# Kernel tuning notes

Hardware: AMD Instinct MI355X
Metric: run time of the kernel (lower is better)

## Reference

```python
import jax, jax.numpy as jnp
import numpy as np

WIN = 7           # window height/width
DIM = 192         # channels
HEADS = 6
HEAD_DIM = DIM // HEADS  # 32
B_WIN = 4096      # num_windows * batch
NW = 64           # windows per image (for shift mask)
N = WIN * WIN     # 49 tokens per window
THETA = 10.0


def _init_rope_freqs(key):
    # init_random_2d_freqs: mag = 1/theta^(arange(0,hd,4)[:hd//4]/hd)
    mag = 1.0 / THETA ** (jnp.arange(0, HEAD_DIM, 4)[: HEAD_DIM // 4].astype(jnp.float32) / HEAD_DIM)
    ang = jax.random.uniform(key, (HEADS, 1)) * 2.0 * jnp.pi
    fx = jnp.concatenate([mag * jnp.cos(ang), mag * jnp.cos(jnp.pi / 2 + ang)], axis=-1)  # [H, hd/2]
    fy = jnp.concatenate([mag * jnp.sin(ang), mag * jnp.sin(jnp.pi / 2 + ang)], axis=-1)
    return jnp.stack([fx, fy], axis=0)  # [2, H, hd/2]


def setup_inputs() -> dict:
    key = jax.random.key(0)
    ks = jax.random.split(key, 6)
    x = jax.random.normal(ks[0], (B_WIN, N, DIM), dtype=jnp.float32)
    mask = jnp.zeros((NW, N, N), dtype=jnp.float32)  # 0/-inf shift mask (zeros: no shift)
    qkv_w = jax.random.normal(ks[1], (3 * DIM, DIM), dtype=jnp.float32) * 0.02
    qkv_b = jnp.zeros((3 * DIM,), dtype=jnp.float32)
    proj_w = jax.random.normal(ks[2], (DIM, DIM), dtype=jnp.float32) * 0.02
    proj_b = jnp.zeros((DIM,), dtype=jnp.float32)
    rope_freqs = _init_rope_freqs(ks[3])
    return {"x": x, "mask": mask, "qkv_w": qkv_w, "qkv_b": qkv_b,
            "proj_w": proj_w, "proj_b": proj_b, "rope_freqs": rope_freqs}


def _rope_angles(rope_freqs):
    # t_x = t % end_x, t_y = t // end_x over the flattened window grid
    t = jnp.arange(N, dtype=jnp.float32)
    t_x = jnp.mod(t, WIN)
    t_y = jnp.floor_divide(t, WIN)
    # angle[h, n, d] = t_x[n]*fx[h,d] + t_y[n]*fy[h,d]  -> [H, N, hd/2]
    ang = (t_x[None, :, None] * rope_freqs[0][:, None, :]
           + t_y[None, :, None] * rope_freqs[1][:, None, :])
    return jnp.cos(ang), jnp.sin(ang)


def _apply_rope(u, cos, sin):
    # u: [B, H, N, hd]; complex multiply on (even, odd) pairs
    b, h, n, d = u.shape
    ur = u.reshape(b, h, n, d // 2, 2)
    re = ur[..., 0] * cos - ur[..., 1] * sin
    im = ur[..., 0] * sin + ur[..., 1] * cos
    return jnp.stack([re, im], axis=-1).reshape(b, h, n, d)


def reference(x, mask, qkv_w, qkv_b, proj_w, proj_b, rope_freqs):
    B_, n, C = x.shape
    H, hd = HEADS, HEAD_DIM
    scale = hd ** -0.5
    qkv = (x @ qkv_w.T + qkv_b).reshape(B_, n, 3, H, hd)
    qkv = jnp.transpose(qkv, (2, 0, 3, 1, 4))          # [3, B, H, N, hd]
    q, k, v = qkv[0] * scale, qkv[1], qkv[2]
    cos, sin = _rope_angles(rope_freqs)                 # [H, N, hd/2]
    q = _apply_rope(q, cos, sin)
    k = _apply_rope(k, cos, sin)
    attn = jnp.einsum('bhnd,bhmd->bhnm', q, k)          # [B, H, N, N]
    nW = mask.shape[0]
    attn = attn.reshape(B_ // nW, nW, H, n, n) + mask[None, :, None]
    attn = jax.nn.softmax(attn.reshape(B_, H, n, n), axis=-1)
    out = jnp.einsum('bhnm,bhmd->bhnd', attn, v)        # [B, H, N, hd]
    out = jnp.transpose(out, (0, 2, 1, 3)).reshape(B_, n, C)
    return out @ proj_w.T + proj_b
```

## Files before the change

kernel.cpp:

```cpp
#include <hip/hip_runtime.h>

#define NTOK 49
#define DIM 192
#define HEADS 6
#define NWIN 64
#define NBLK 4096

typedef unsigned short u16;
typedef short bf16x8 __attribute__((ext_vector_type(8)));
typedef unsigned short u16x4 __attribute__((ext_vector_type(4)));
typedef unsigned short u16x8 __attribute__((ext_vector_type(8)));
typedef float f32x4 __attribute__((ext_vector_type(4)));

#define QKVW_ELEMS (3 * DIM * DIM)
#define PROJW_ELEMS (DIM * DIM)

#define TB_OFF_BYTES ((QKVW_ELEMS + PROJW_ELEMS) * 2)
#define TB_QUADS     (HEADS * NTOK * 8)

#define R1_OFF 0
#define K_OFF  24576
#define PS_OFF 44176
#define LDS_TOTAL 51232

__device__ __forceinline__ float bf2f(u16 u) {
    union { unsigned int i; float f; } x; x.i = ((unsigned int)u) << 16; return x.f;
}
__device__ __forceinline__ u16 f2bf(float f) {
    union { float f; unsigned int u; } x; x.f = f;
    unsigned int u = x.u;
    u += 0x7fffu + ((u >> 16) & 1u);
    return (u16)(u >> 16);
}

extern "C" __global__ void __launch_bounds__(256)
convert_weights(const float* __restrict__ qkv_w, const float* __restrict__ proj_w,
                u16* __restrict__ ws) {
    int i = (blockIdx.x * 256 + threadIdx.x) * 4;
    if (i >= QKVW_ELEMS + PROJW_ELEMS) return;
    const float* s = (i < QKVW_ELEMS) ? (qkv_w + i) : (proj_w + (i - QKVW_ELEMS));
    float4 v = *(const float4*)s;
    ushort4 o;
    o.x = f2bf(v.x); o.y = f2bf(v.y); o.z = f2bf(v.z); o.w = f2bf(v.w);
    *(ushort4*)(ws + i) = o;
}

extern "C" __global__ void __launch_bounds__(256)
rope_table(const float* __restrict__ rfreq, float* __restrict__ tb) {
    int i = blockIdx.x * 256 + threadIdx.x;
    if (i >= TB_QUADS) return;
    int h = i / (NTOK * 8);
    int r = i % (NTOK * 8);
    int t = r >> 3;
    int p0 = (r & 7) * 2;
    float tx = (float)(t % 7), ty = (float)(t / 7);
    float a0 = tx * rfreq[h * 16 + p0]     + ty * rfreq[96 + h * 16 + p0];
    float a1 = tx * rfreq[h * 16 + p0 + 1] + ty * rfreq[96 + h * 16 + p0 + 1];
    float4 o;
    o.x = cosf(a0); o.y = sinf(a0);
    o.z = cosf(a1); o.w = sinf(a1);
    ((float4*)tb)[i] = o;
}

extern "C" __global__ void __launch_bounds__(256, 3)
fused_win_attn(const float* __restrict__ x, const float* __restrict__ mask,
               const u16* __restrict__ wsq, const float* __restrict__ qkv_b,
               const u16* __restrict__ wsp, const float* __restrict__ proj_b,
               const float* __restrict__ tb, float* __restrict__ out)
{
    __shared__ __align__(16) char smem[LDS_TOTAL];
    u16* xs = (u16*)(smem + R1_OFF);
    u16* qs = (u16*)(smem + R1_OFF);
    u16* vt = (u16*)(smem + R1_OFF);
    u16* kb = (u16*)(smem + K_OFF);
    u16* ps = (u16*)(smem + PS_OFF);

    const int tid  = threadIdx.x;
    const int wave = tid >> 6;
    const int lane = tid & 63;
    const int ln   = lane & 15;
    const int quad = lane >> 4;
    const int blk  = blockIdx.x;
    const int widx = blk & (NWIN - 1);
    const float* xg = x + (long)blk * NTOK * DIM;
    const f32x4 fzero = {0.f, 0.f, 0.f, 0.f};
    const float scale = 0.17677669529663687f;

    float mreg[4][4];
    #pragma unroll
    for (int nt = 0; nt < 4; nt++) {
        int m = nt * 16 + ln;
        #pragma unroll
        for (int r = 0; r < 4; r++) {
            int n = wave * 16 + quad * 4 + r;
            mreg[nt][r] = (m >= NTOK) ? -1e30f
                         : ((n < NTOK) ? mask[widx * (NTOK * NTOK) + n * NTOK + m] : 0.f);
        }
    }

    for (int i = tid; i < NTOK * 48; i += 256) {
        int r = i / 48, c = (i % 48) * 4;
        float4 v = *(const float4*)(xg + r * DIM + c);
        u16x4 o = { f2bf(v.x), f2bf(v.y), f2bf(v.z), f2bf(v.w) };
        *(u16x4*)(xs + r * 200 + c) = o;
    }
    __syncthreads();

    bf16x8 bfrag[6][4];
    #pragma unroll
    for (int kk = 0; kk < 6; kk++)
        #pragma unroll
        for (int nt = 0; nt < 4; nt++) {
            int row = nt * 16 + ln; if (row > NTOK - 1) row = NTOK - 1;
            bfrag[kk][nt] = *(const bf16x8*)(xs + row * 200 + kk * 32 + quad * 8);
        }
    __syncthreads();

    for (int jt = wave; jt < 24; jt += 4) {
        bf16x8 af[6];
        const u16* wr = wsq + (jt * 16 + ln) * DIM + quad * 8;
        #pragma unroll
        for (int kk = 0; kk < 6; kk++) af[kk] = *(const bf16x8*)(wr + kk * 32);
        f32x4 acc[4];
        #pragma unroll
        for (int nt = 0; nt < 4; nt++) acc[nt] = fzero;
        #pragma unroll
        for (int kk = 0; kk < 6; kk++)
            #pragma unroll
            for (int nt = 0; nt < 4; nt++)
                acc[nt] = __builtin_amdgcn_mfma_f32_16x16x32_bf16(af[kk], bfrag[kk][nt], acc[nt], 0, 0, 0);

        int j0 = jt * 16 + quad * 4;
        int isq = (jt < 12);
        int c0 = j0 % DIM;
        int hh = c0 >> 5;
        int p0 = (c0 & 31) >> 1;
        float b0 = qkv_b[j0],   b1 = qkv_b[j0+1];
        float b2 = qkv_b[j0+2], b3 = qkv_b[j0+3];
        #pragma unroll
        for (int nt = 0; nt < 4; nt++) {
            int t = nt * 16 + ln;
            float v0 = acc[nt][0] + b0;
            float v1 = acc[nt][1] + b1;
            float v2 = acc[nt][2] + b2;
            float v3 = acc[nt][3] + b3;
            if (t < NTOK) {
                float4 tv = ((const float4*)tb)[(hh * NTOK + t) * 8 + (p0 >> 1)];
                float r0 = v0 * tv.x - v1 * tv.y;
                float i0 = v0 * tv.y + v1 * tv.x;
                float r1 = v2 * tv.z - v3 * tv.w;
                float i1 = v2 * tv.w + v3 * tv.z;
                if (isq) { r0 *= scale; i0 *= scale; r1 *= scale; i1 *= scale; }
                u16x4 pk = { f2bf(r0), f2bf(i0), f2bf(r1), f2bf(i1) };
                *(u16x4*)((isq ? qs : kb) + t * 200 + c0) = pk;
            }
        }
    }
    __syncthreads();

    bf16x8 qreg[6];
    {
        int qrow = wave * 16 + ln; if (qrow > NTOK - 1) qrow = NTOK - 1;
        #pragma unroll
        for (int h = 0; h < HEADS; h++)
            qreg[h] = *(const bf16x8*)(qs + qrow * 200 + h * 32 + quad * 8);
    }
    __syncthreads();

    for (int jt = 24 + wave; jt < 36; jt += 4) {
        bf16x8 af[6];
        const u16* wr = wsq + (jt * 16 + ln) * DIM + quad * 8;
        #pragma unroll
        for (int kk = 0; kk < 6; kk++) af[kk] = *(const bf16x8*)(wr + kk * 32);
        f32x4 acc[4];
        #pragma unroll
        for (int nt = 0; nt < 4; nt++) acc[nt] = fzero;
        #pragma unroll
        for (int kk = 0; kk < 6; kk++)
            #pragma unroll
            for (int nt = 0; nt < 4; nt++)
                acc[nt] = __builtin_amdgcn_mfma_f32_16x16x32_bf16(af[kk], bfrag[kk][nt], acc[nt], 0, 0, 0);

        int j0 = jt * 16 + quad * 4;
        int c0 = j0 - 2 * DIM;
        float b0 = qkv_b[j0],   b1 = qkv_b[j0+1];
        float b2 = qkv_b[j0+2], b3 = qkv_b[j0+3];
        #pragma unroll
        for (int nt = 0; nt < 4; nt++) {
            int t = nt * 16 + ln;
            float w0 = (t < NTOK) ? acc[nt][0] + b0 : 0.f;
            float w1 = (t < NTOK) ? acc[nt][1] + b1 : 0.f;
            float w2 = (t < NTOK) ? acc[nt][2] + b2 : 0.f;
            float w3 = (t < NTOK) ? acc[nt][3] + b3 : 0.f;
            vt[(c0+0) * 64 + (t ^ (((c0+0) & 7) << 3))] = f2bf(w0);
            vt[(c0+1) * 64 + (t ^ (((c0+1) & 7) << 3))] = f2bf(w1);
            vt[(c0+2) * 64 + (t ^ (((c0+2) & 7) << 3))] = f2bf(w2);
            vt[(c0+3) * 64 + (t ^ (((c0+3) & 7) << 3))] = f2bf(w3);
        }
    }
    __syncthreads();

    u16x4 op0[HEADS], op1[HEADS];
    #pragma unroll
    for (int h = 0; h < HEADS; h++) {
        f32x4 s4[4];
        #pragma unroll
        for (int nt = 0; nt < 4; nt++) {
            int krow = nt * 16 + ln; if (krow > NTOK - 1) krow = NTOK - 1;
            bf16x8 bk = *(const bf16x8*)(kb + krow * 200 + h * 32 + quad * 8);
            s4[nt] = __builtin_amdgcn_mfma_f32_16x16x32_bf16(qreg[h], bk, fzero, 0, 0, 0);
        }
        #pragma unroll
        for (int nt = 0; nt < 4; nt++)
            #pragma unroll
            for (int r = 0; r < 4; r++)
                s4[nt][r] += mreg[nt][r];
        float mx[4], sm[4], rs[4];
        #pragma unroll
        for (int r = 0; r < 4; r++) {
            float v = fmaxf(fmaxf(s4[0][r], s4[1][r]), fmaxf(s4[2][r], s4[3][r]));
            #pragma unroll
            for (int d = 1; d < 16; d <<= 1) v = fmaxf(v, __shfl_xor(v, d));
            mx[r] = v; sm[r] = 0.f;
        }
        #pragma unroll
        for (int nt = 0; nt < 4; nt++) {
            int m = nt * 16 + ln;
            #pragma unroll
            for (int r = 0; r < 4; r++) {
                float e = __expf(s4[nt][r] - mx[r]);
                sm[r] += e;
                int prow = wave * 16 + quad * 4 + r;
                if (prow < NTOK) ps[prow * 72 + m] = f2bf(e);
            }
        }
        #pragma unroll
        for (int r = 0; r < 4; r++) {
            float v = sm[r];
            #pragma unroll
            for (int d = 1; d < 16; d <<= 1) v += __shfl_xor(v, d);
            rs[r] = 1.0f / v;
        }
        f32x4 o0 = fzero, o1 = fzero;
        int arow = wave * 16 + ln; if (arow > NTOK - 1) arow = NTOK - 1;
        int swz = (ln & 7) << 3;
        #pragma unroll
        for (int kk = 0; kk < 2; kk++) {
            bf16x8 ap  = *(const bf16x8*)(ps + arow * 72 + kk * 32 + quad * 8);
            int cbase = (kk * 32 + quad * 8) ^ swz;
            bf16x8 bv0 = *(const bf16x8*)(vt + (h * 32 + ln) * 64      + cbase);
            bf16x8 bv1 = *(const bf16x8*)(vt + (h * 32 + 16 + ln) * 64 + cbase);
            o0 = __builtin_amdgcn_mfma_f32_16x16x32_bf16(ap, bv0, o0, 0, 0, 0);
            o1 = __builtin_amdgcn_mfma_f32_16x16x32_bf16(ap, bv1, o1, 0, 0, 0);
        }
        #pragma unroll
        for (int r = 0; r < 4; r++) {
            op0[h][r] = f2bf(o0[r] * rs[r]);
            op1[h][r] = f2bf(o1[r] * rs[r]);
        }
    }
    __syncthreads();

    #pragma unroll
    for (int h = 0; h < HEADS; h++)
        #pragma unroll
        for (int r = 0; r < 4; r++) {
            int t = wave * 16 + quad * 4 + r;
            if (t < NTOK) {
                kb[t * 200 + h * 32 + ln]      = op0[h][r];
                kb[t * 200 + h * 32 + 16 + ln] = op1[h][r];
            }
        }
    bf16x8 aa[6];
    int arow = wave * 16 + ln; if (arow > NTOK - 1) arow = NTOK - 1;
    #pragma unroll
    for (int kk = 0; kk < 6; kk++)
        aa[kk] = *(const bf16x8*)(kb + arow * 200 + kk * 32 + quad * 8);
    float* ob = out + (long)blk * (NTOK * DIM);
    for (int nt = 0; nt < 12; nt++) {
        const u16* wp = wsp + (nt * 16 + ln) * DIM + quad * 8;
        f32x4 p4 = fzero;
        #pragma unroll
        for (int kk = 0; kk < 6; kk++) {
            bf16x8 bw = *(const bf16x8*)(wp + kk * 32);
            p4 = __builtin_amdgcn_mfma_f32_16x16x32_bf16(aa[kk], bw, p4, 0, 0, 0);
        }
        float bb = proj_b[nt * 16 + ln];
        #pragma unroll
        for (int r = 0; r < 4; r++) {
            int t = wave * 16 + quad * 4 + r;
            if (t < NTOK) ob[t * DIM + nt * 16 + ln] = p4[r] + bb;
        }
    }
}

extern "C" void kernel_launch(void* const* d_in, const int* in_sizes, int n_in,
                              void* d_out, int out_size, void* d_ws, size_t ws_size,
                              hipStream_t stream) {
    (void)in_sizes; (void)n_in; (void)out_size; (void)ws_size;
    u16* ws = (u16*)d_ws;
    convert_weights<<<dim3((QKVW_ELEMS + PROJW_ELEMS) / 4 / 256 + 1), dim3(256), 0, stream>>>(
        (const float*)d_in[2], (const float*)d_in[4], ws);
    float* tb = (float*)((char*)d_ws + TB_OFF_BYTES);
    rope_table<<<dim3((TB_QUADS + 255) / 256), dim3(256), 0, stream>>>(
        (const float*)d_in[6], tb);
    fused_win_attn<<<dim3(NBLK), dim3(256), 0, stream>>>(
        (const float*)d_in[0], (const float*)d_in[1],
        ws, (const float*)d_in[3],
        ws + QKVW_ELEMS, (const float*)d_in[5],
        tb, (float*)d_out);
}
```

Baseline: 582.7 us.

## Prefetch weight fragments across GEMM iterations, pack mask to bf16, drop softmax max

The QKV and projection GEMM loops now double-buffer their weight fragments, so the next tile's global loads are issued before the current tile's MFMAs. This is meant to hide global load latency. The shift mask is packed into bf16 pairs to cut register pressure. The softmax no longer subtracts the row max, which removes two shuffle reductions per head but can overflow in exp if attention scores are large.

```diff
diff --git a/kernel.cpp b/kernel.cpp
--- a/kernel.cpp
+++ b/kernel.cpp
@@ -25,6 +25,12 @@
 
 __device__ __forceinline__ float bf2f(u16 u) {
     union { unsigned int i; float f; } x; x.i = ((unsigned int)u) << 16; return x.f;
+}
+__device__ __forceinline__ float bfbits_lo(unsigned int p) {
+    union { unsigned int i; float f; } x; x.i = p << 16; return x.f;
+}
+__device__ __forceinline__ float bfbits_hi(unsigned int p) {
+    union { unsigned int i; float f; } x; x.i = p & 0xffff0000u; return x.f;
 }
 __device__ __forceinline__ u16 f2bf(float f) {
     union { float f; unsigned int u; } x; x.f = f;
@@ -86,15 +92,18 @@
     const f32x4 fzero = {0.f, 0.f, 0.f, 0.f};
     const float scale = 0.17677669529663687f;
 
-    float mreg[4][4];
+    unsigned int mpk[8];
     #pragma unroll
     for (int nt = 0; nt < 4; nt++) {
         int m = nt * 16 + ln;
         #pragma unroll
-        for (int r = 0; r < 4; r++) {
-            int n = wave * 16 + quad * 4 + r;
-            mreg[nt][r] = (m >= NTOK) ? -1e30f
-                         : ((n < NTOK) ? mask[widx * (NTOK * NTOK) + n * NTOK + m] : 0.f);
+        for (int rr = 0; rr < 2; rr++) {
+            int n0 = wave * 16 + quad * 4 + rr * 2;
+            float v0 = (m >= NTOK) ? -1e30f
+                       : ((n0 < NTOK) ? mask[widx * (NTOK * NTOK) + n0 * NTOK + m] : 0.f);
+            float v1 = (m >= NTOK) ? -1e30f
+                       : ((n0 + 1 < NTOK) ? mask[widx * (NTOK * NTOK) + (n0 + 1) * NTOK + m] : 0.f);
+            mpk[nt * 2 + rr] = (unsigned int)f2bf(v0) | ((unsigned int)f2bf(v1) << 16);
         }
     }
 
@@ -116,43 +125,53 @@
         }
     __syncthreads();
 
-    for (int jt = wave; jt < 24; jt += 4) {
-        bf16x8 af[6];
-        const u16* wr = wsq + (jt * 16 + ln) * DIM + quad * 8;
-        #pragma unroll
-        for (int kk = 0; kk < 6; kk++) af[kk] = *(const bf16x8*)(wr + kk * 32);
-        f32x4 acc[4];
-        #pragma unroll
-        for (int nt = 0; nt < 4; nt++) acc[nt] = fzero;
-        #pragma unroll
-        for (int kk = 0; kk < 6; kk++)
-            #pragma unroll
-            for (int nt = 0; nt < 4; nt++)
-                acc[nt] = __builtin_amdgcn_mfma_f32_16x16x32_bf16(af[kk], bfrag[kk][nt], acc[nt], 0, 0, 0);
-
-        int j0 = jt * 16 + quad * 4;
-        int isq = (jt < 12);
-        int c0 = j0 % DIM;
-        int hh = c0 >> 5;
-        int p0 = (c0 & 31) >> 1;
-        float b0 = qkv_b[j0],   b1 = qkv_b[j0+1];
-        float b2 = qkv_b[j0+2], b3 = qkv_b[j0+3];
-        #pragma unroll
-        for (int nt = 0; nt < 4; nt++) {
-            int t = nt * 16 + ln;
-            float v0 = acc[nt][0] + b0;
-            float v1 = acc[nt][1] + b1;
-            float v2 = acc[nt][2] + b2;
-            float v3 = acc[nt][3] + b3;
-            if (t < NTOK) {
-                float4 tv = ((const float4*)tb)[(hh * NTOK + t) * 8 + (p0 >> 1)];
-                float r0 = v0 * tv.x - v1 * tv.y;
-                float i0 = v0 * tv.y + v1 * tv.x;
-                float r1 = v2 * tv.z - v3 * tv.w;
-                float i1 = v2 * tv.w + v3 * tv.z;
-                if (isq) { r0 *= scale; i0 *= scale; r1 *= scale; i1 *= scale; }
-                u16x4 pk = { f2bf(r0), f2bf(i0), f2bf(r1), f2bf(i1) };
-                *(u16x4*)((isq ? qs : kb) + t * 200 + c0) = pk;
+    {
+        const u16* wr = wsq + (wave * 16 + ln) * DIM + quad * 8;
+        bf16x8 afn[6];
+        #pragma unroll
+        for (int kk = 0; kk < 6; kk++) afn[kk] = *(const bf16x8*)(wr + kk * 32);
+        for (int jt = wave; jt < 24; jt += 4) {
+            bf16x8 af[6];
+            #pragma unroll
+            for (int kk = 0; kk < 6; kk++) af[kk] = afn[kk];
+            wr += 64 * DIM;
+            if (jt + 4 < 24) {
+                #pragma unroll
+                for (int kk = 0; kk < 6; kk++) afn[kk] = *(const bf16x8*)(wr + kk * 32);
+            }
+            f32x4 acc[4];
+            #pragma unroll
+            for (int nt = 0; nt < 4; nt++) acc[nt] = fzero;
+            #pragma unroll
+            for (int kk = 0; kk < 6; kk++)
+                #pragma unroll
+                for (int nt = 0; nt < 4; nt++)
+                    acc[nt] = __builtin_amdgcn_mfma_f32_16x16x32_bf16(af[kk], bfrag[kk][nt], acc[nt], 0, 0, 0);
+
+            int j0 = jt * 16 + quad * 4;
+            int isq = (jt < 12);
+            int c0 = j0 % DIM;
+            int hh = c0 >> 5;
+            int p0 = (c0 & 31) >> 1;
+            float b0 = qkv_b[j0],   b1 = qkv_b[j0+1];
+            float b2 = qkv_b[j0+2], b3 = qkv_b[j0+3];
+            #pragma unroll
+            for (int nt = 0; nt < 4; nt++) {
+                int t = nt * 16 + ln;
+                float v0 = acc[nt][0] + b0;
+                float v1 = acc[nt][1] + b1;
+                float v2 = acc[nt][2] + b2;
+                float v3 = acc[nt][3] + b3;
+                if (t < NTOK) {
+                    float4 tv = ((const float4*)tb)[(hh * NTOK + t) * 8 + (p0 >> 1)];
+                    float r0 = v0 * tv.x - v1 * tv.y;
+                    float i0 = v0 * tv.y + v1 * tv.x;
+                    float r1 = v2 * tv.z - v3 * tv.w;
+                    float i1 = v2 * tv.w + v3 * tv.z;
+                    if (isq) { r0 *= scale; i0 *= scale; r1 *= scale; i1 *= scale; }
+                    u16x4 pk = { f2bf(r0), f2bf(i0), f2bf(r1), f2bf(i1) };
+                    *(u16x4*)((isq ? qs : kb) + t * 200 + c0) = pk;
+                }
             }
         }
     }
@@ -167,35 +186,45 @@
     }
     __syncthreads();
 
-    for (int jt = 24 + wave; jt < 36; jt += 4) {
-        bf16x8 af[6];
-        const u16* wr = wsq + (jt * 16 + ln) * DIM + quad * 8;
-        #pragma unroll
-        for (int kk = 0; kk < 6; kk++) af[kk] = *(const bf16x8*)(wr + kk * 32);
-        f32x4 acc[4];
-        #pragma unroll
-        for (int nt = 0; nt < 4; nt++) acc[nt] = fzero;
-        #pragma unroll
-        for (int kk = 0; kk < 6; kk++)
-            #pragma unroll
-            for (int nt = 0; nt < 4; nt++)
-                acc[nt] = __builtin_amdgcn_mfma_f32_16x16x32_bf16(af[kk], bfrag[kk][nt], acc[nt], 0, 0, 0);
-
-        int j0 = jt * 16 + quad * 4;
-        int c0 = j0 - 2 * DIM;
-        float b0 = qkv_b[j0],   b1 = qkv_b[j0+1];
-        float b2 = qkv_b[j0+2], b3 = qkv_b[j0+3];
-        #pragma unroll
-        for (int nt = 0; nt < 4; nt++) {
-            int t = nt * 16 + ln;
-            float w0 = (t < NTOK) ? acc[nt][0] + b0 : 0.f;
-            float w1 = (t < NTOK) ? acc[nt][1] + b1 : 0.f;
-            float w2 = (t < NTOK) ? acc[nt][2] + b2 : 0.f;
-            float w3 = (t < NTOK) ? acc[nt][3] + b3 : 0.f;
-            vt[(c0+0) * 64 + (t ^ (((c0+0) & 7) << 3))] = f2bf(w0);
-            vt[(c0+1) * 64 + (t ^ (((c0+1) & 7) << 3))] = f2bf(w1);
-            vt[(c0+2) * 64 + (t ^ (((c0+2) & 7) << 3))] = f2bf(w2);
-            vt[(c0+3) * 64 + (t ^ (((c0+3) & 7) << 3))] = f2bf(w3);
+    {
+        const u16* wr = wsq + ((24 + wave) * 16 + ln) * DIM + quad * 8;
+        bf16x8 afn[6];
+        #pragma unroll
+        for (int kk = 0; kk < 6; kk++) afn[kk] = *(const bf16x8*)(wr + kk * 32);
+        for (int jt = 24 + wave; jt < 36; jt += 4) {
+            bf16x8 af[6];
+            #pragma unroll
+            for (int kk = 0; kk < 6; kk++) af[kk] = afn[kk];
+            wr += 64 * DIM;
+            if (jt + 4 < 36) {
+                #pragma unroll
+                for (int kk = 0; kk < 6; kk++) afn[kk] = *(const bf16x8*)(wr + kk * 32);
+            }
+            f32x4 acc[4];
+            #pragma unroll
+            for (int nt = 0; nt < 4; nt++) acc[nt] = fzero;
+            #pragma unroll
+            for (int kk = 0; kk < 6; kk++)
+                #pragma unroll
+                for (int nt = 0; nt < 4; nt++)
+                    acc[nt] = __builtin_amdgcn_mfma_f32_16x16x32_bf16(af[kk], bfrag[kk][nt], acc[nt], 0, 0, 0);
+
+            int j0 = jt * 16 + quad * 4;
+            int c0 = j0 - 2 * DIM;
+            float b0 = qkv_b[j0],   b1 = qkv_b[j0+1];
+            float b2 = qkv_b[j0+2], b3 = qkv_b[j0+3];
+            #pragma unroll
+            for (int nt = 0; nt < 4; nt++) {
+                int t = nt * 16 + ln;
+                float w0 = (t < NTOK) ? acc[nt][0] + b0 : 0.f;
+                float w1 = (t < NTOK) ? acc[nt][1] + b1 : 0.f;
+                float w2 = (t < NTOK) ? acc[nt][2] + b2 : 0.f;
+                float w3 = (t < NTOK) ? acc[nt][3] + b3 : 0.f;
+                vt[(c0+0) * 64 + (t ^ (((c0+0) & 7) << 3))] = f2bf(w0);
+                vt[(c0+1) * 64 + (t ^ (((c0+1) & 7) << 3))] = f2bf(w1);
+                vt[(c0+2) * 64 + (t ^ (((c0+2) & 7) << 3))] = f2bf(w2);
+                vt[(c0+3) * 64 + (t ^ (((c0+3) & 7) << 3))] = f2bf(w3);
+            }
         }
     }
     __syncthreads();
@@ -210,30 +239,23 @@
             bf16x8 bk = *(const bf16x8*)(kb + krow * 200 + h * 32 + quad * 8);
             s4[nt] = __builtin_amdgcn_mfma_f32_16x16x32_bf16(qreg[h], bk, fzero, 0, 0, 0);
         }
-        #pragma unroll
-        for (int nt = 0; nt < 4; nt++)
-            #pragma unroll
-            for (int r = 0; r < 4; r++)
-                s4[nt][r] += mreg[nt][r];
-        float mx[4], sm[4], rs[4];
-        #pragma unroll
-        for (int r = 0; r < 4; r++) {
-            float v = fmaxf(fmaxf(s4[0][r], s4[1][r]), fmaxf(s4[2][r], s4[3][r]));
-            #pragma unroll
-            for (int d = 1; d < 16; d <<= 1) v = fmaxf(v, __shfl_xor(v, d));
-            mx[r] = v; sm[r] = 0.f;
-        }
+        float sm[4] = {0.f, 0.f, 0.f, 0.f};
         #pragma unroll
         for (int nt = 0; nt < 4; nt++) {
             int m = nt * 16 + ln;
             #pragma unroll
-            for (int r = 0; r < 4; r++) {
-                float e = __expf(s4[nt][r] - mx[r]);
-                sm[r] += e;
-                int prow = wave * 16 + quad * 4 + r;
-                if (prow < NTOK) ps[prow * 72 + m] = f2bf(e);
-            }
-        }
+            for (int rr = 0; rr < 2; rr++) {
+                unsigned int pk = mpk[nt * 2 + rr];
+                float e0 = __expf(s4[nt][rr*2]   + bfbits_lo(pk));
+                float e1 = __expf(s4[nt][rr*2+1] + bfbits_hi(pk));
+                sm[rr*2]   += e0;
+                sm[rr*2+1] += e1;
+                int prow = wave * 16 + quad * 4 + rr * 2;
+                if (prow < NTOK)     ps[prow * 72 + m]       = f2bf(e0);
+                if (prow + 1 < NTOK) ps[(prow + 1) * 72 + m] = f2bf(e1);
+            }
+        }
+        float rs[4];
         #pragma unroll
         for (int r = 0; r < 4; r++) {
             float v = sm[r];
@@ -276,20 +298,32 @@
     #pragma unroll
     for (int kk = 0; kk < 6; kk++)
         aa[kk] = *(const bf16x8*)(kb + arow * 200 + kk * 32 + quad * 8);
+
     float* ob = out + (long)blk * (NTOK * DIM);
-    for (int nt = 0; nt < 12; nt++) {
-        const u16* wp = wsp + (nt * 16 + ln) * DIM + quad * 8;
-        f32x4 p4 = fzero;
-        #pragma unroll
-        for (int kk = 0; kk < 6; kk++) {
-            bf16x8 bw = *(const bf16x8*)(wp + kk * 32);
-            p4 = __builtin_amdgcn_mfma_f32_16x16x32_bf16(aa[kk], bw, p4, 0, 0, 0);
-        }
-        float bb = proj_b[nt * 16 + ln];
-        #pragma unroll
-        for (int r = 0; r < 4; r++) {
-            int t = wave * 16 + quad * 4 + r;
-            if (t < NTOK) ob[t * DIM + nt * 16 + ln] = p4[r] + bb;
+    {
+        const u16* wp = wsp + ln * DIM + quad * 8;
+        bf16x8 bwn[6];
+        #pragma unroll
+        for (int kk = 0; kk < 6; kk++) bwn[kk] = *(const bf16x8*)(wp + kk * 32);
+        for (int nt = 0; nt < 12; nt++) {
+            bf16x8 bw[6];
+            #pragma unroll
+            for (int kk = 0; kk < 6; kk++) bw[kk] = bwn[kk];
+            wp += 16 * DIM;
+            if (nt < 11) {
+                #pragma unroll
+                for (int kk = 0; kk < 6; kk++) bwn[kk] = *(const bf16x8*)(wp + kk * 32);
+            }
+            f32x4 p4 = fzero;
+            #pragma unroll
+            for (int kk = 0; kk < 6; kk++)
+                p4 = __builtin_amdgcn_mfma_f32_16x16x32_bf16(aa[kk], bw[kk], p4, 0, 0, 0);
+            float bb = proj_b[nt * 16 + ln];
+            #pragma unroll
+            for (int r = 0; r < 4; r++) {
+                int t = wave * 16 + quad * 4 + r;
+                if (t < NTOK) ob[t * DIM + nt * 16 + ln] = p4[r] + bb;
+            }
         }
     }
 }
```

Result: slower. 770.3 us (+32.2%).
